# Optimization experiments

Measured on AMD Instinct MI355X. Metric: run time of the kernel, lower is better.

The kernel has to match this reference:

```python
import jax, jax.numpy as jnp
import numpy as np

B, D, F, H = 256, 9, 8, 256   # batch of trees, tree depth, input features, hidden
N = 2 ** (D + 1) - 1          # total nodes per full binary tree (heap layout)


def _init(key, shape, fan_in):
    return jax.random.normal(key, shape, jnp.float32) * (1.0 / np.sqrt(fan_in))


def setup_inputs() -> dict:
    key = jax.random.key(0)
    ks = jax.random.split(key, 6)
    return {
        "data": jax.random.normal(ks[0], (B, N, F), jnp.float32),
        "Wu": _init(ks[1], (H, F), F),
        "bu": jnp.zeros((H,), jnp.float32),
        "Wr": _init(ks[2], (3 * H, 3 * H), 3 * H),
        "br": jnp.zeros((3 * H,), jnp.float32),
        "Wh": _init(ks[3], (H, 3 * H), 3 * H),
        "bh": jnp.zeros((H,), jnp.float32),
        "Wz": _init(ks[4], (4 * H, 4 * H), 4 * H),
        "bz": jnp.zeros((4 * H,), jnp.float32),
        "Wp": _init(ks[5], (1, H), H),
        "bp": jnp.zeros((1,), jnp.float32),
    }


def reference(data, Wu, bu, Wr, br, Wh, bh, Wz, bz, Wp, bp):
    # data: [B, N, F] node features in heap (level-order) layout;
    # children of the i-th node of level l are nodes 2i, 2i+1 of level l+1.
    b, n_nodes, _ = data.shape
    L = (n_nodes + 1) // 2          # number of leaves
    depth = L.bit_length() - 1
    h_dim = Wu.shape[0]

    # leaf embedding u for every node (leaf() is applied at every tree node)
    u = jnp.einsum('bnf,hf->bnh', data, Wu) + bu          # [B, N, H]
    h = u[:, L - 1:, :]                                    # leaf level states [B, L, H]

    for l in range(depth - 1, -1, -1):                     # bottom-up over levels
        n = 2 ** l
        parent = u[:, n - 1:2 * n - 1, :]                  # [B, n, H]
        h_l, h_r = h[:, 0::2, :], h[:, 1::2, :]            # [B, n, H] each
        hhu = jnp.concatenate([parent, h_l, h_r], axis=-1)  # [B, n, 3H]
        r = jax.nn.sigmoid(jnp.einsum('bnk,jk->bnj', hhu, Wr) + br)
        h_new = jax.nn.relu(jnp.einsum('bnk,hk->bnh', r * hhu, Wh) + bh)
        hhhu = jnp.concatenate([h_new, hhu], axis=-1)      # [B, n, 4H]
        zlin = jnp.einsum('bnk,jk->bnj', hhhu, Wz) + bz    # [B, n, 4H]
        z = jax.nn.softmax(zlin.reshape(b, n, 4, h_dim), axis=2)
        h = (z * hhhu.reshape(b, n, 4, h_dim)).sum(axis=2)  # gated combine -> [B, n, H]

    # h is [B, 1, H] at the root; logits head
    logits = jnp.einsum('bnh,oh->bno', h, Wp) + bp          # [B, 1, 1]
    return logits[:, 0, 0]                                  # [B]
```

## Files before the change

### kernel.cpp

```cpp
#include <hip/hip_runtime.h>
#include <math.h>

#define BB 256
#define NN 1023
#define FF 8
#define HH 256
#define DEPTH 9

enum { EPI_NONE = 0, EPI_SIGMUL = 1, EPI_RELU = 2, EPI_COMBINE = 3 };

typedef __bf16 bf16x8_t __attribute__((ext_vector_type(8)));
typedef __bf16 bf16x4_t __attribute__((ext_vector_type(4)));
typedef float f32x4_t __attribute__((ext_vector_type(4)));

__device__ __forceinline__ void stage16(const void* g, void* l) {
    __builtin_amdgcn_global_load_lds(
        (const __attribute__((address_space(1))) void*)g,
        (__attribute__((address_space(3))) void*)l,
        16, 0, 0);
}

template <int EPI>
__global__ __launch_bounds__(256) void gemm_mfma(
    const __bf16* __restrict__ A, int lda,
    const __bf16* __restrict__ W,
    const float* __restrict__ bias,
    const __bf16* __restrict__ aux, int ldaux,
    void* __restrict__ Cout, int ldc,
    int K)
{
    __shared__ __bf16 As[128 * 32];
    __shared__ __bf16 Bs[128 * 32];
    const int tid = threadIdx.x;
    const int lane = tid & 63;
    const int w = tid >> 6;
    const int wr = w >> 1, wc = w & 1;

    const int nwg = gridDim.x * gridDim.y;
    const int hw = blockIdx.y * gridDim.x + blockIdx.x;
    const int xcd = hw & 7, k0 = hw >> 3;
    const int qq = nwg >> 3, rr = nwg & 7;
    const int wg = (xcd < rr ? xcd * (qq + 1) : rr * (qq + 1) + (xcd - rr) * qq) + k0;
    const int bm0 = (wg / gridDim.x) * 128;
    const int bn0 = (wg % gridDim.x) * 128;

    const int srow = lane >> 2;
    const int scol = (lane & 3) * 8;

    f32x4_t acc[4][4];
#pragma unroll
    for (int i = 0; i < 4; ++i)
#pragma unroll
        for (int j = 0; j < 4; ++j) acc[i][j] = (f32x4_t){0.f, 0.f, 0.f, 0.f};

    const int rA = lane & 15;
    const int kslot = (lane >> 4) * 8;

    for (int kk = 0; kk < K; kk += 32) {
        stage16(A + (size_t)(bm0 + w * 16 + srow) * lda + kk + scol,
                &As[(w * 16) * 32]);
        stage16(A + (size_t)(bm0 + 64 + w * 16 + srow) * lda + kk + scol,
                &As[(64 + w * 16) * 32]);
        stage16(W + (size_t)(bn0 + w * 16 + srow) * K + kk + scol,
                &Bs[(w * 16) * 32]);
        stage16(W + (size_t)(bn0 + 64 + w * 16 + srow) * K + kk + scol,
                &Bs[(64 + w * 16) * 32]);
        __syncthreads();

        bf16x8_t af[4], bfr[4];
#pragma unroll
        for (int i = 0; i < 4; ++i)
            af[i] = *(const bf16x8_t*)&As[(wr * 64 + i * 16 + rA) * 32 + kslot];
#pragma unroll
        for (int j = 0; j < 4; ++j)
            bfr[j] = *(const bf16x8_t*)&Bs[(wc * 64 + j * 16 + rA) * 32 + kslot];
#pragma unroll
        for (int i = 0; i < 4; ++i)
#pragma unroll
            for (int j = 0; j < 4; ++j)
                acc[i][j] = __builtin_amdgcn_mfma_f32_16x16x32_bf16(
                    af[i], bfr[j], acc[i][j], 0, 0, 0);
        __syncthreads();
    }

    if (EPI == EPI_COMBINE) {
        const int r = lane & 15;
        const int G = ((bn0 + wc * 64) >> 2) + r;
        float bz4[4];
#pragma unroll
        for (int g = 0; g < 4; ++g) bz4[g] = bias[bn0 + wc * 64 + g * 16 + r];
#pragma unroll
        for (int i = 0; i < 4; ++i) {
#pragma unroll
            for (int reg = 0; reg < 4; ++reg) {
                const int gr = bm0 + wr * 64 + i * 16 + (lane >> 4) * 4 + reg;
                float z0 = acc[i][0][reg] + bz4[0];
                float z1 = acc[i][1][reg] + bz4[1];
                float z2 = acc[i][2][reg] + bz4[2];
                float z3 = acc[i][3][reg] + bz4[3];
                float mx = fmaxf(fmaxf(z0, z1), fmaxf(z2, z3));
                float e0 = __expf(z0 - mx), e1 = __expf(z1 - mx);
                float e2 = __expf(z2 - mx), e3 = __expf(z3 - mx);
                const __bf16* hrow = aux + (size_t)gr * ldaux + G;
                float hv = (e0 * (float)hrow[0] + e1 * (float)hrow[256] +
                            e2 * (float)hrow[512] + e3 * (float)hrow[768]) /
                           (e0 + e1 + e2 + e3);
                ((__bf16*)Cout)[(size_t)gr * ldc + G] = (__bf16)hv;
            }
        }
    } else {
        const int rowbase = bm0 + wr * 64;
        const int colbase = bn0 + wc * 64;
#pragma unroll
        for (int j = 0; j < 4; ++j) {
            const int gc = colbase + j * 16 + (lane & 15);
            const float bv = bias[gc];
#pragma unroll
            for (int i = 0; i < 4; ++i) {
#pragma unroll
                for (int reg = 0; reg < 4; ++reg) {
                    const int gr = rowbase + i * 16 + (lane >> 4) * 4 + reg;
                    float v = acc[i][j][reg] + bv;
                    if (EPI == EPI_SIGMUL) {
                        float s = 1.0f / (1.0f + __expf(-v));
                        v = s * (float)aux[(size_t)gr * ldaux + gc];
                        ((__bf16*)Cout)[(size_t)gr * ldc + gc] = (__bf16)v;
                    } else if (EPI == EPI_RELU) {
                        v = fmaxf(v, 0.0f);
                        ((__bf16*)Cout)[(size_t)gr * ldc + gc] = (__bf16)v;
                    } else {
                        ((float*)Cout)[(size_t)gr * ldc + gc] = v;
                    }
                }
            }
        }
    }
}

__global__ __launch_bounds__(256) void convert_weights(
    const float* __restrict__ Wr, const float* __restrict__ Wh,
    const float* __restrict__ Wz, const float* __restrict__ bz,
    __bf16* __restrict__ Wrb, __bf16* __restrict__ Whb,
    __bf16* __restrict__ Wzb, float* __restrict__ bzp)
{
    const int NR = 768 * 768, NH2 = 256 * 768, NZ = 1024 * 1024;
    const int idx0 = blockIdx.x * 256 + threadIdx.x;
    for (int i = idx0; i < NR + NH2 + NZ; i += gridDim.x * 256) {
        if (i < NR) Wrb[i] = (__bf16)Wr[i];
        else if (i < NR + NH2) Whb[i - NR] = (__bf16)Wh[i - NR];
        else {
            const int z = i - NR - NH2;
            const int p = z >> 10, k = z & 1023;
            const int o = ((p >> 4) & 3) * 256 + (p >> 6) * 16 + (p & 15);
            Wzb[z] = (__bf16)Wz[(size_t)o * 1024 + k];
        }
    }
    if (idx0 < 1024) {
        const int p = idx0;
        const int o = ((p >> 4) & 3) * 256 + (p >> 6) * 16 + (p & 15);
        bzp[p] = bz[o];
    }
}

__global__ __launch_bounds__(256) void leaves_kernel(
    const float* __restrict__ data, const float* __restrict__ Wu,
    const float* __restrict__ bu, __bf16* __restrict__ h0)
{
    const int row = blockIdx.x * 4 + (threadIdx.x >> 6);
    const int c0 = (threadIdx.x & 63) * 4;
    const int b = row >> 9, j = row & 511;
    const float* d = data + ((size_t)b * NN + 511 + j) * FF;
    float dv[8];
#pragma unroll
    for (int f = 0; f < FF; ++f) dv[f] = d[f];
    bf16x4_t o;
#pragma unroll
    for (int cc = 0; cc < 4; ++cc) {
        const int h = c0 + cc;
        float acc = bu[h];
#pragma unroll
        for (int f = 0; f < FF; ++f) acc += dv[f] * Wu[h * FF + f];
        o[cc] = (__bf16)acc;
    }
    *(bf16x4_t*)&h0[(size_t)row * HH + c0] = o;
}

__global__ __launch_bounds__(256) void build_hhu(
    const float* __restrict__ data, const float* __restrict__ Wu,
    const float* __restrict__ bu, const __bf16* __restrict__ hprev,
    __bf16* __restrict__ hhhu, int l, int r0)
{
    const int n = 1 << l;
    const int row = blockIdx.x * 4 + (threadIdx.x >> 6);
    const int c0 = (threadIdx.x & 63) * 4;
    const int i = r0 + row;
    const int b = i >> l;
    const int m = i & (n - 1);

    const float* d = data + ((size_t)b * NN + (n - 1) + m) * FF;
    float dv[8];
#pragma unroll
    for (int f = 0; f < FF; ++f) dv[f] = d[f];

    __bf16* rowp = hhhu + (size_t)row * 1024;
    bf16x4_t o;
#pragma unroll
    for (int cc = 0; cc < 4; ++cc) {
        const int h = c0 + cc;
        float acc = bu[h];
#pragma unroll
        for (int f = 0; f < FF; ++f) acc += dv[f] * Wu[h * FF + f];
        o[cc] = (__bf16)acc;
    }
    *(bf16x4_t*)&rowp[256 + c0] = o;
    *(bf16x4_t*)&rowp[512 + c0] =
        *(const bf16x4_t*)&hprev[((size_t)b * (2 * n) + 2 * m) * HH + c0];
    *(bf16x4_t*)&rowp[768 + c0] =
        *(const bf16x4_t*)&hprev[((size_t)b * (2 * n) + 2 * m + 1) * HH + c0];
}

__global__ __launch_bounds__(256) void final_kernel(
    const __bf16* __restrict__ hfin, const float* __restrict__ Wp,
    const float* __restrict__ bp, float* __restrict__ out)
{
    const int b = blockIdx.x;
    const int t = threadIdx.x;
    __shared__ float red[256];
    red[t] = (float)hfin[(size_t)b * HH + t] * Wp[t];
    __syncthreads();
    for (int s = 128; s > 0; s >>= 1) {
        if (t < s) red[t] += red[t + s];
        __syncthreads();
    }
    if (t == 0) out[b] = red[0] + bp[0];
}

extern "C" void kernel_launch(void* const* d_in, const int* in_sizes, int n_in,
                              void* d_out, int out_size, void* d_ws, size_t ws_size,
                              hipStream_t stream)
{
    const float* data = (const float*)d_in[0];
    const float* Wu = (const float*)d_in[1];
    const float* bu = (const float*)d_in[2];
    const float* Wr = (const float*)d_in[3];
    const float* br = (const float*)d_in[4];
    const float* Wh = (const float*)d_in[5];
    const float* bh = (const float*)d_in[6];
    const float* Wz = (const float*)d_in[7];
    const float* bz = (const float*)d_in[8];
    const float* Wp = (const float*)d_in[9];
    const float* bp = (const float*)d_in[10];
    float* out = (float*)d_out;

    const size_t CAP = 32768;
    char* w = (char*)d_ws;
    __bf16* hA = (__bf16*)w;   w += (size_t)BB * 512 * HH * 2;
    __bf16* hB = (__bf16*)w;   w += (size_t)BB * 256 * HH * 2;
    __bf16* hhhu = (__bf16*)w; w += CAP * 1024 * 2;
    __bf16* rh = (__bf16*)w;   w += CAP * 768 * 2;
    __bf16* Wrb = (__bf16*)w;  w += (size_t)768 * 768 * 2;
    __bf16* Whb = (__bf16*)w;  w += (size_t)256 * 768 * 2;
    __bf16* Wzb = (__bf16*)w;  w += (size_t)1024 * 1024 * 2;
    float* bzp = (float*)w;    w += 1024 * 4;

    convert_weights<<<2048, 256, 0, stream>>>(Wr, Wh, Wz, bz, Wrb, Whb, Wzb, bzp);
    leaves_kernel<<<BB * 512 / 4, 256, 0, stream>>>(data, Wu, bu, hA);

    __bf16* hprev = hA;
    __bf16* hnext = hB;
    for (int l = DEPTH - 1; l >= 0; --l) {
        const size_t M = (size_t)BB << l;
        for (size_t r0 = 0; r0 < M; r0 += CAP) {
            const int R = (int)((M - r0 < CAP) ? (M - r0) : CAP);
            build_hhu<<<R / 4, 256, 0, stream>>>(data, Wu, bu, hprev, hhhu, l, (int)r0);
            dim3 g1(768 / 128, R / 128);
            gemm_mfma<EPI_SIGMUL><<<g1, 256, 0, stream>>>(
                hhhu + 256, 1024, Wrb, br, hhhu + 256, 1024, rh, 768, 768);
            dim3 g2(256 / 128, R / 128);
            gemm_mfma<EPI_RELU><<<g2, 256, 0, stream>>>(
                rh, 768, Whb, bh, nullptr, 0, hhhu, 1024, 768);
            dim3 g3(1024 / 128, R / 128);
            gemm_mfma<EPI_COMBINE><<<g3, 256, 0, stream>>>(
                hhhu, 1024, Wzb, bzp, hhhu, 1024,
                hnext + (size_t)r0 * HH, HH, 1024);
        }
        __bf16* t = hprev; hprev = hnext; hnext = t;
    }
    final_kernel<<<BB, 256, 0, stream>>>(hprev, Wp, bp, out);
}
```

Before: 1.397 ms.

## Add 256x256 tiled MFMA GEMM with XCD remap and fuse leaf embedding

Adds a 512-thread GEMM kernel that uses 256x256 tiles, double-buffered LDS staging and an XCD-aware workgroup remap. It is used for the large-M chunks of the Wr and Wz GEMMs to raise data reuse per block. The separate leaf-embedding kernel is removed and leaf embeddings are computed inside build_hhu at the bottom level. build_hhu is also vectorized to 8 columns per thread with weights held in registers. The large tile uses 128KB of LDS and many accumulators, which limits occupancy.

```diff
diff --git a/kernel.cpp b/kernel.cpp
--- a/kernel.cpp
+++ b/kernel.cpp
@@ -18,6 +18,136 @@
         (const __attribute__((address_space(1))) void*)g,
         (__attribute__((address_space(3))) void*)l,
         16, 0, 0);
+}
+
+template <int EPI>
+__global__ __launch_bounds__(512) void gemm256(
+    const __bf16* __restrict__ A, int lda,
+    const __bf16* __restrict__ W,
+    const float* __restrict__ bias,
+    const __bf16* __restrict__ aux, int ldaux,
+    void* __restrict__ Cout, int ldc,
+    int K)
+{
+    __shared__ __bf16 lds[2][2][256 * 64];
+    const int tid = threadIdx.x;
+    const int lane = tid & 63;
+    const int w = tid >> 6;
+    const int wr = w >> 2, wc = w & 3;
+
+    const int nwg = gridDim.x * gridDim.y;
+    const int hw = blockIdx.y * gridDim.x + blockIdx.x;
+    const int xcd = hw & 7, k0 = hw >> 3;
+    const int qq = nwg >> 3, rr = nwg & 7;
+    const int wg = (xcd < rr ? xcd * (qq + 1) : rr * (qq + 1) + (xcd - rr) * qq) + k0;
+    const int bm0 = (wg / gridDim.x) * 256;
+    const int bn0 = (wg % gridDim.x) * 256;
+
+    const int srow = tid >> 3;
+    const int scol = (tid & 7) * 8;
+
+    f32x4_t acc[8][4];
+#pragma unroll
+    for (int i = 0; i < 8; ++i)
+#pragma unroll
+        for (int j = 0; j < 4; ++j) acc[i][j] = (f32x4_t){0.f, 0.f, 0.f, 0.f};
+
+    const int rA = lane & 15;
+    const int klane = (lane >> 4) * 8;
+    const int NT = K >> 6;
+
+#pragma unroll
+    for (int p = 0; p < 4; ++p) {
+        stage16(A + (size_t)(bm0 + p * 64 + srow) * lda + scol,
+                &lds[0][0][p * 4096 + w * 512]);
+        stage16(W + (size_t)(bn0 + p * 64 + srow) * K + scol,
+                &lds[0][1][p * 4096 + w * 512]);
+    }
+    __syncthreads();
+
+    for (int kt = 0; kt < NT; ++kt) {
+        const int cur = kt & 1;
+        if (kt + 1 < NT) {
+            const int kk = (kt + 1) << 6;
+#pragma unroll
+            for (int p = 0; p < 4; ++p) {
+                stage16(A + (size_t)(bm0 + p * 64 + srow) * lda + kk + scol,
+                        &lds[cur ^ 1][0][p * 4096 + w * 512]);
+                stage16(W + (size_t)(bn0 + p * 64 + srow) * K + kk + scol,
+                        &lds[cur ^ 1][1][p * 4096 + w * 512]);
+            }
+        }
+        const __bf16* As = lds[cur][0];
+        const __bf16* Bs = lds[cur][1];
+#pragma unroll
+        for (int ks = 0; ks < 2; ++ks) {
+            bf16x8_t af[8], bfr[4];
+#pragma unroll
+            for (int i = 0; i < 8; ++i)
+                af[i] = *(const bf16x8_t*)&As[(wr * 128 + i * 16 + rA) * 64 + ks * 32 + klane];
+#pragma unroll
+            for (int j = 0; j < 4; ++j)
+                bfr[j] = *(const bf16x8_t*)&Bs[(wc * 64 + j * 16 + rA) * 64 + ks * 32 + klane];
+#pragma unroll
+            for (int i = 0; i < 8; ++i)
+#pragma unroll
+                for (int j = 0; j < 4; ++j)
+                    acc[i][j] = __builtin_amdgcn_mfma_f32_16x16x32_bf16(
+                        af[i], bfr[j], acc[i][j], 0, 0, 0);
+        }
+        __syncthreads();
+    }
+
+    if (EPI == EPI_COMBINE) {
+        const int r = lane & 15;
+        const int G = ((bn0 + wc * 64) >> 2) + r;
+        float bz4[4];
+#pragma unroll
+        for (int g = 0; g < 4; ++g) bz4[g] = bias[bn0 + wc * 64 + g * 16 + r];
+#pragma unroll
+        for (int i = 0; i < 8; ++i) {
+#pragma unroll
+            for (int reg = 0; reg < 4; ++reg) {
+                const int gr = bm0 + wr * 128 + i * 16 + (lane >> 4) * 4 + reg;
+                float z0 = acc[i][0][reg] + bz4[0];
+                float z1 = acc[i][1][reg] + bz4[1];
+                float z2 = acc[i][2][reg] + bz4[2];
+                float z3 = acc[i][3][reg] + bz4[3];
+                float mx = fmaxf(fmaxf(z0, z1), fmaxf(z2, z3));
+                float e0 = __expf(z0 - mx), e1 = __expf(z1 - mx);
+                float e2 = __expf(z2 - mx), e3 = __expf(z3 - mx);
+                const __bf16* hrow = aux + (size_t)gr * ldaux + G;
+                float hv = (e0 * (float)hrow[0] + e1 * (float)hrow[256] +
+                            e2 * (float)hrow[512] + e3 * (float)hrow[768]) /
+                           (e0 + e1 + e2 + e3);
+                ((__bf16*)Cout)[(size_t)gr * ldc + G] = (__bf16)hv;
+            }
+        }
+    } else {
+#pragma unroll
+        for (int j = 0; j < 4; ++j) {
+            const int gc = bn0 + wc * 64 + j * 16 + (lane & 15);
+            const float bv = bias[gc];
+#pragma unroll
+            for (int i = 0; i < 8; ++i) {
+#pragma unroll
+                for (int reg = 0; reg < 4; ++reg) {
+                    const int gr = bm0 + wr * 128 + i * 16 + (lane >> 4) * 4 + reg;
+                    float v = acc[i][j][reg] + bv;
+                    if (EPI == EPI_SIGMUL) {
+                        float s = 1.0f / (1.0f + __expf(-v));
+                        v = s * (float)aux[(size_t)gr * ldaux + gc];
+                        ((__bf16*)Cout)[(size_t)gr * ldc + gc] = (__bf16)v;
+                    } else if (EPI == EPI_RELU) {
+                        v = fmaxf(v, 0.0f);
+                        ((__bf16*)Cout)[(size_t)gr * ldc + gc] = (__bf16)v;
+                    } else {
+                        ((float*)Cout)[(size_t)gr * ldc + gc] = v;
+                    }
+                }
+            }
+        }
+    }
 }
 
 template <int EPI>
@@ -109,17 +239,15 @@
             }
         }
     } else {
-        const int rowbase = bm0 + wr * 64;
-        const int colbase = bn0 + wc * 64;
 #pragma unroll
         for (int j = 0; j < 4; ++j) {
-            const int gc = colbase + j * 16 + (lane & 15);
+            const int gc = bn0 + wc * 64 + j * 16 + (lane & 15);
             const float bv = bias[gc];
 #pragma unroll
             for (int i = 0; i < 4; ++i) {
 #pragma unroll
                 for (int reg = 0; reg < 4; ++reg) {
-                    const int gr = rowbase + i * 16 + (lane >> 4) * 4 + reg;
+                    const int gr = bm0 + wr * 64 + i * 16 + (lane >> 4) * 4 + reg;
                     float v = acc[i][j][reg] + bv;
                     if (EPI == EPI_SIGMUL) {
                         float s = 1.0f / (1.0f + __expf(-v));
@@ -162,61 +290,70 @@
     }
 }
 
-__global__ __launch_bounds__(256) void leaves_kernel(
-    const float* __restrict__ data, const float* __restrict__ Wu,
-    const float* __restrict__ bu, __bf16* __restrict__ h0)
-{
-    const int row = blockIdx.x * 4 + (threadIdx.x >> 6);
-    const int c0 = (threadIdx.x & 63) * 4;
-    const int b = row >> 9, j = row & 511;
-    const float* d = data + ((size_t)b * NN + 511 + j) * FF;
-    float dv[8];
-#pragma unroll
-    for (int f = 0; f < FF; ++f) dv[f] = d[f];
-    bf16x4_t o;
-#pragma unroll
-    for (int cc = 0; cc < 4; ++cc) {
-        const int h = c0 + cc;
-        float acc = bu[h];
-#pragma unroll
-        for (int f = 0; f < FF; ++f) acc += dv[f] * Wu[h * FF + f];
-        o[cc] = (__bf16)acc;
-    }
-    *(bf16x4_t*)&h0[(size_t)row * HH + c0] = o;
-}
-
 __global__ __launch_bounds__(256) void build_hhu(
     const float* __restrict__ data, const float* __restrict__ Wu,
     const float* __restrict__ bu, const __bf16* __restrict__ hprev,
     __bf16* __restrict__ hhhu, int l, int r0)
 {
     const int n = 1 << l;
-    const int row = blockIdx.x * 4 + (threadIdx.x >> 6);
-    const int c0 = (threadIdx.x & 63) * 4;
+    const int row = blockIdx.x * 8 + (threadIdx.x >> 5);
+    const int c0 = (threadIdx.x & 31) * 8;
     const int i = r0 + row;
     const int b = i >> l;
     const int m = i & (n - 1);
 
-    const float* d = data + ((size_t)b * NN + (n - 1) + m) * FF;
-    float dv[8];
-#pragma unroll
-    for (int f = 0; f < FF; ++f) dv[f] = d[f];
+    float wv[8][8];
+#pragma unroll
+    for (int cc = 0; cc < 8; ++cc) {
+        float4 w0 = *(const float4*)&Wu[(c0 + cc) * 8];
+        float4 w1 = *(const float4*)&Wu[(c0 + cc) * 8 + 4];
+        wv[cc][0] = w0.x; wv[cc][1] = w0.y; wv[cc][2] = w0.z; wv[cc][3] = w0.w;
+        wv[cc][4] = w1.x; wv[cc][5] = w1.y; wv[cc][6] = w1.z; wv[cc][7] = w1.w;
+    }
+    float buv[8];
+#pragma unroll
+    for (int cc = 0; cc < 8; ++cc) buv[cc] = bu[c0 + cc];
 
     __bf16* rowp = hhhu + (size_t)row * 1024;
-    bf16x4_t o;
-#pragma unroll
-    for (int cc = 0; cc < 4; ++cc) {
-        const int h = c0 + cc;
-        float acc = bu[h];
-#pragma unroll
-        for (int f = 0; f < FF; ++f) acc += dv[f] * Wu[h * FF + f];
-        o[cc] = (__bf16)acc;
-    }
-    *(bf16x4_t*)&rowp[256 + c0] = o;
-    *(bf16x4_t*)&rowp[512 + c0] =
-        *(const bf16x4_t*)&hprev[((size_t)b * (2 * n) + 2 * m) * HH + c0];
-    *(bf16x4_t*)&rowp[768 + c0] =
-        *(const bf16x4_t*)&hprev[((size_t)b * (2 * n) + 2 * m + 1) * HH + c0];
+
+    {
+        const float* dp = data + ((size_t)b * NN + (n - 1) + m) * FF;
+        float4 d0 = *(const float4*)dp, d1 = *(const float4*)(dp + 4);
+        float dv[8] = {d0.x, d0.y, d0.z, d0.w, d1.x, d1.y, d1.z, d1.w};
+        bf16x8_t o;
+#pragma unroll
+        for (int cc = 0; cc < 8; ++cc) {
+            float acc = buv[cc];
+#pragma unroll
+            for (int f = 0; f < 8; ++f) acc += dv[f] * wv[cc][f];
+            o[cc] = (__bf16)acc;
+        }
+        *(bf16x8_t*)&rowp[256 + c0] = o;
+    }
+
+    if (l == 8) {
+        const float* dl = data + ((size_t)b * NN + 511 + 2 * m) * FF;
+#pragma unroll
+        for (int side = 0; side < 2; ++side) {
+            const float* dp = dl + side * FF;
+            float4 d0 = *(const float4*)dp, d1 = *(const float4*)(dp + 4);
+            float dv[8] = {d0.x, d0.y, d0.z, d0.w, d1.x, d1.y, d1.z, d1.w};
+            bf16x8_t o;
+#pragma unroll
+            for (int cc = 0; cc < 8; ++cc) {
+                float acc = buv[cc];
+#pragma unroll
+                for (int f = 0; f < 8; ++f) acc += dv[f] * wv[cc][f];
+                o[cc] = (__bf16)acc;
+            }
+            *(bf16x8_t*)&rowp[512 + side * 256 + c0] = o;
+        }
+    } else {
+        *(bf16x8_t*)&rowp[512 + c0] =
+            *(const bf16x8_t*)&hprev[((size_t)b * (2 * n) + 2 * m) * HH + c0];
+        *(bf16x8_t*)&rowp[768 + c0] =
+            *(const bf16x8_t*)&hprev[((size_t)b * (2 * n) + 2 * m + 1) * HH + c0];
+    }
 }
 
 __global__ __launch_bounds__(256) void final_kernel(
@@ -254,8 +391,8 @@
 
     const size_t CAP = 32768;
     char* w = (char*)d_ws;
-    __bf16* hA = (__bf16*)w;   w += (size_t)BB * 512 * HH * 2;
-    __bf16* hB = (__bf16*)w;   w += (size_t)BB * 256 * HH * 2;
+    __bf16* hA = (__bf16*)w;   w += (size_t)65536 * HH * 2;
+    __bf16* hB = (__bf16*)w;   w += (size_t)32768 * HH * 2;
     __bf16* hhhu = (__bf16*)w; w += CAP * 1024 * 2;
     __bf16* rh = (__bf16*)w;   w += CAP * 768 * 2;
     __bf16* Wrb = (__bf16*)w;  w += (size_t)768 * 768 * 2;
@@ -264,27 +401,33 @@
     float* bzp = (float*)w;    w += 1024 * 4;
 
     convert_weights<<<2048, 256, 0, stream>>>(Wr, Wh, Wz, bz, Wrb, Whb, Wzb, bzp);
-    leaves_kernel<<<BB * 512 / 4, 256, 0, stream>>>(data, Wu, bu, hA);
-
-    __bf16* hprev = hA;
-    __bf16* hnext = hB;
+
     for (int l = DEPTH - 1; l >= 0; --l) {
         const size_t M = (size_t)BB << l;
+        __bf16* dst = ((DEPTH - 1 - l) & 1) ? hB : hA;
+        const __bf16* src = ((DEPTH - 1 - l) & 1) ? hA : hB;
         for (size_t r0 = 0; r0 < M; r0 += CAP) {
             const int R = (int)((M - r0 < CAP) ? (M - r0) : CAP);
-            build_hhu<<<R / 4, 256, 0, stream>>>(data, Wu, bu, hprev, hhhu, l, (int)r0);
-            dim3 g1(768 / 128, R / 128);
-            gemm_mfma<EPI_SIGMUL><<<g1, 256, 0, stream>>>(
-                hhhu + 256, 1024, Wrb, br, hhhu + 256, 1024, rh, 768, 768);
-            dim3 g2(256 / 128, R / 128);
-            gemm_mfma<EPI_RELU><<<g2, 256, 0, stream>>>(
+            build_hhu<<<R / 8, 256, 0, stream>>>(data, Wu, bu, src, hhhu, l, (int)r0);
+            if (R >= 32768) {
+                gemm256<EPI_SIGMUL><<<dim3(3, R / 256), 512, 0, stream>>>(
+                    hhhu + 256, 1024, Wrb, br, hhhu + 256, 1024, rh, 768, 768);
+            } else {
+                gemm_mfma<EPI_SIGMUL><<<dim3(6, R / 128), 256, 0, stream>>>(
+                    hhhu + 256, 1024, Wrb, br, hhhu + 256, 1024, rh, 768, 768);
+            }
+            gemm_mfma<EPI_RELU><<<dim3(2, R / 128), 256, 0, stream>>>(
                 rh, 768, Whb, bh, nullptr, 0, hhhu, 1024, 768);
-            dim3 g3(1024 / 128, R / 128);
-            gemm_mfma<EPI_COMBINE><<<g3, 256, 0, stream>>>(
-                hhhu, 1024, Wzb, bzp, hhhu, 1024,
-                hnext + (size_t)r0 * HH, HH, 1024);
-        }
-        __bf16* t = hprev; hprev = hnext; hnext = t;
-    }
-    final_kernel<<<BB, 256, 0, stream>>>(hprev, Wp, bp, out);
-}
+            if (R >= 16384) {
+                gemm256<EPI_COMBINE><<<dim3(4, R / 256), 512, 0, stream>>>(
+                    hhhu, 1024, Wzb, bzp, hhhu, 1024,
+                    dst + (size_t)r0 * HH, HH, 1024);
+            } else {
+                gemm_mfma<EPI_COMBINE><<<dim3(8, R / 128), 256, 0, stream>>>(
+                    hhhu, 1024, Wzb, bzp, hhhu, 1024,
+                    dst + (size_t)r0 * HH, HH, 1024);
+            }
+        }
+    }
+    final_kernel<<<BB, 256, 0, stream>>>(hA, Wp, bp, out);
+}
```

After: 1.252 ms. 1.12x faster.
